# Kernel tuning notes

Measured on AMD Instinct MI355X. Metric: run time of the kernel, lower is better.

Reference implementation:

```python
import jax, jax.numpy as jnp
import numpy as np

# Config (matches init_kwargs)
B, T, N = 32, 512, 1024
FT, FS = 16, 32                 # max_time_F, max_space_F
NCH = FT * FS                   # n_channels = 512
MULT = 2
DIN = NCH * MULT                # input_dim = 1024
H = 1024                        # hidden_size
NCLS = 1                        # n_cls_tokens
NP = (T // FT) * (N // FS)      # n_patches = 1024
SCALE = float(H) ** 0.5         # config.scale is None -> hidden_size**0.5


def setup_inputs() -> dict:
    key = jax.random.key(0)
    k0, k1, k2, k3 = jax.random.split(key, 4)
    s = 0.02
    return {
        "spikes": jax.random.normal(k0, (B, T, N), dtype=jnp.float32),
        "W_embed": jax.random.normal(k1, (DIN, NCH), dtype=jnp.float32) * s,
        "b_embed": jnp.zeros((DIN,), dtype=jnp.float32),
        "cls_tokens": jnp.zeros((1, NCLS, DIN), dtype=jnp.float32),
        "W_proj": jax.random.normal(k2, (H, DIN), dtype=jnp.float32) * s,
        "b_proj": jnp.zeros((H,), dtype=jnp.float32),
        "pos_table": jax.random.normal(k3, (NP + NCLS, H), dtype=jnp.float32) * s,
    }


def reference(spikes, W_embed, b_embed, cls_tokens, W_proj, b_proj, pos_table):
    Bsz = spikes.shape[0]
    # Patchify: replaces the double python loop with one reshape/transpose.
    # [B,T,N] -> [B, T/FT, FT, N/FS, FS] -> [B, T/FT, N/FS, FT, FS] -> [B, NP, NCH]
    # flatten order (time-major within patch) matches torch's .flatten(1) on [B,FT,FS].
    patches = spikes.reshape(Bsz, T // FT, FT, N // FS, FS)
    patches = patches.transpose(0, 1, 3, 2, 4).reshape(Bsz, NP, NCH)
    # embed_spikes (linear)
    x = jnp.einsum("bpc,dc->bpd", patches, W_embed) + b_embed
    # prepend cls tokens
    cls = jnp.broadcast_to(cls_tokens, (Bsz, NCLS, DIN))
    x = jnp.concatenate([cls, x], axis=1)
    # act * scale, then projection
    x = jax.nn.gelu(x, approximate=False) * SCALE
    x = jnp.einsum("bpd,hd->bph", x, W_proj) + b_proj
    # positional embedding: stamps are arange, so direct table add
    stamp = jnp.broadcast_to(
        jnp.arange(NP + NCLS, dtype=jnp.int32)[None, :], (Bsz, NP + NCLS)
    )
    mask = jnp.ones((Bsz, NP + NCLS), dtype=jnp.int32)
    x = x + pos_table[None, :, :]
    # dropout p=0.0 -> identity
    return (x, mask, stamp)
```

## Files before the change

### kernel.cpp

```cpp
#include <hip/hip_runtime.h>
#include <stdint.h>


typedef __attribute__((ext_vector_type(8))) short bf16x8;
typedef __attribute__((ext_vector_type(4))) float f32x4;

#define VMCNT(n) asm volatile("s_waitcnt vmcnt(" #n ")" ::: "memory")
#define CFENCE() asm volatile("" ::: "memory")

__device__ __forceinline__ unsigned short f2bf(float f) {
  union { float f; unsigned u; } v; v.f = f;
  const unsigned u = v.u;
  return (unsigned short)((u + 0x7fffu + ((u >> 16) & 1u)) >> 16);
}

__device__ __forceinline__ float gelu_exact(float x) {
  return 0.5f * x * (1.0f + erff(x * 0.70710678118654752440f));
}

__device__ __forceinline__ void gl_lds16(const unsigned short* g, unsigned short* l) {
  __builtin_amdgcn_global_load_lds(
      (const __attribute__((address_space(1))) unsigned int*)g,
      (__attribute__((address_space(3))) unsigned int*)l, 16, 0, 0);
}


__global__ void cast_f32_bf16(const float* __restrict__ src,
                              unsigned short* __restrict__ dst, int n) {
  const int i = blockIdx.x * 256 + threadIdx.x;
  if (i < n) dst[i] = f2bf(src[i]);
}

__global__ void patchify(const float* __restrict__ spikes,
                         unsigned short* __restrict__ P) {
  const int idx = blockIdx.x * 256 + threadIdx.x;
  const int m = idx >> 7;
  const int c = (idx & 127) << 2;
  const int b = m >> 10, p = m & 1023;
  const int pt = p >> 5, ps = p & 31;
  const int ft = c >> 5, fs = c & 31;
  const float4 v = *(const float4*)(spikes +
      (size_t)(((b << 9) + pt * 16 + ft) << 10) + ps * 32 + fs);
  ushort4 o;
  o.x = f2bf(v.x); o.y = f2bf(v.y); o.z = f2bf(v.z); o.w = f2bf(v.w);
  *(ushort4*)(P + (size_t)m * 512 + c) = o;
}

__global__ void g0_and_pad(const float* __restrict__ cls,
                           unsigned short* __restrict__ G) {
  const int i = blockIdx.x * 256 + threadIdx.x;
  G[(size_t)32800 * 1024 + i] = 0;
  if (i < 1024) {
    const unsigned short bv = f2bf(gelu_exact(cls[i]) * 32.0f);
    for (int b = 0; b < 32; ++b) G[(size_t)(b * 1025) * 1024 + i] = bv;
  }
}

__global__ void mask_stamp(float* __restrict__ out) {
  const int i = blockIdx.x * 256 + threadIdx.x;
  if (i < 32800) {
    out[33587200 + i] = 1.0f;
    out[33587200 + 32800 + i] = (float)(i % 1025);
  }
}

__device__ __forceinline__ void stage_tile(
    const unsigned short* __restrict__ A, const unsigned short* __restrict__ B,
    int K, int rowStart, int colStart, int k0, int g0,
    unsigned short* la, unsigned short* lb) {
#pragma unroll
  for (int s = 0; s < 4; ++s) {
    const int g = g0 + s * 64;
    const int r = g >> 3;
    const int slot = g & 7;
    const int kc = (slot ^ (r & 7)) << 3;
    gl_lds16(A + (size_t)(rowStart + r) * K + (k0 + kc), la + r * 64 + slot * 8);
    gl_lds16(B + (size_t)(colStart + r) * K + (k0 + kc), lb + r * 64 + slot * 8);
  }
}

template <int K, bool GELU_EPI, int ROWBLKS>
__global__ __launch_bounds__(256) void gemm_bt(
    const unsigned short* __restrict__ A, const unsigned short* __restrict__ B,
    const float* __restrict__ bias, unsigned short* __restrict__ Cg,
    float* __restrict__ Cf, const float* __restrict__ pos, int Mvalid) {
  __shared__ __align__(16) unsigned short lsA[2][128 * 64];
  __shared__ __align__(16) unsigned short lsB[2][128 * 64];
  constexpr int NT = K / 64;

  const int tid = threadIdx.x;
  const int lane = tid & 63;
  const int w = tid >> 6;
  const int quad = lane >> 4;
  const int l16 = lane & 15;

  const int L = blockIdx.x;
  const int xcd = L & 7;
  const int j = L >> 3;
  int rowBlk, colBlk;
  if (ROWBLKS > 256 && j >= 256) { rowBlk = 256; colBlk = xcd; }
  else { rowBlk = xcd * 32 + (j >> 3); colBlk = j & 7; }
  const int rowStart = rowBlk * 128;
  const int colStart = colBlk * 128;
  const int wm = (w >> 1) * 64;
  const int wn = (w & 1) * 64;

  f32x4 acc[4][4];
  const f32x4 z = {0.f, 0.f, 0.f, 0.f};
#pragma unroll
  for (int i = 0; i < 4; ++i)
#pragma unroll
    for (int j2 = 0; j2 < 4; ++j2) acc[i][j2] = z;

  const int g0 = w * 256 + lane;

  stage_tile(A, B, K, rowStart, colStart, 0, g0, lsA[0], lsB[0]);

  for (int t = 0; t < NT; ++t) {
    const int cur = t & 1;
    if (t + 1 < NT) {
      stage_tile(A, B, K, rowStart, colStart, (t + 1) * 64, g0,
                 lsA[cur ^ 1], lsB[cur ^ 1]);
      VMCNT(8);
    } else {
      VMCNT(0);
    }
    __builtin_amdgcn_s_barrier();
    CFENCE();

    const unsigned short* cA = lsA[cur];
    const unsigned short* cB = lsB[cur];
#pragma unroll
    for (int kk = 0; kk < 64; kk += 32) {
      bf16x8 af[4], bfr[4];
      const int kcb = (kk >> 3) + quad;
#pragma unroll
      for (int i = 0; i < 4; ++i) {
        const int r = wm + i * 16 + l16;
        af[i] = *(const bf16x8*)(cA + r * 64 + ((kcb ^ (r & 7)) << 3));
      }
#pragma unroll
      for (int j2 = 0; j2 < 4; ++j2) {
        const int r = wn + j2 * 16 + l16;
        bfr[j2] = *(const bf16x8*)(cB + r * 64 + ((kcb ^ (r & 7)) << 3));
      }
#pragma unroll
      for (int i = 0; i < 4; ++i)
#pragma unroll
        for (int j2 = 0; j2 < 4; ++j2)
          acc[i][j2] = __builtin_amdgcn_mfma_f32_16x16x32_bf16(af[i], bfr[j2],
                                                               acc[i][j2], 0, 0, 0);
    }

    CFENCE();
    __builtin_amdgcn_s_barrier();
    CFENCE();
  }

#pragma unroll
  for (int i = 0; i < 4; ++i) {
    const int rb = rowStart + wm + i * 16 + quad * 4;
#pragma unroll
    for (int j2 = 0; j2 < 4; ++j2) {
      const int gc = colStart + wn + j2 * 16 + l16;
      const float bv = bias[gc];
#pragma unroll
      for (int r = 0; r < 4; ++r) {
        const int row = rb + r;
        float v = acc[i][j2][r] + bv;
        if (GELU_EPI) {
          v = gelu_exact(v) * 32.0f;
          const int grow = row + (row >> 10) + 1;
          Cg[(size_t)grow * 1024 + gc] = f2bf(v);
        } else {
          if (row < Mvalid) {
            const int p = row % 1025;
            Cf[(size_t)row * 1024 + gc] = v + pos[(size_t)p * 1024 + gc];
          }
        }
      }
    }
  }
}


extern "C" void kernel_launch(void* const* d_in, const int* in_sizes, int n_in,
                              void* d_out, int out_size, void* d_ws, size_t ws_size,
                              hipStream_t stream) {
  const float* spikes  = (const float*)d_in[0];
  const float* W_embed = (const float*)d_in[1];
  const float* b_embed = (const float*)d_in[2];
  const float* cls     = (const float*)d_in[3];
  const float* W_proj  = (const float*)d_in[4];
  const float* b_proj  = (const float*)d_in[5];
  const float* pos     = (const float*)d_in[6];
  float* out = (float*)d_out;

  char* ws = (char*)d_ws;
  unsigned short* P  = (unsigned short*)(ws);
  unsigned short* G  = (unsigned short*)(ws + 33554432);
  unsigned short* WE = (unsigned short*)(ws + 100925440);
  unsigned short* WP = (unsigned short*)(ws + 101974016);

  hipLaunchKernelGGL(cast_f32_bf16, dim3(2048), dim3(256), 0, stream, W_embed, WE, 524288);
  hipLaunchKernelGGL(cast_f32_bf16, dim3(4096), dim3(256), 0, stream, W_proj, WP, 1048576);
  hipLaunchKernelGGL(patchify, dim3(16384), dim3(256), 0, stream, spikes, P);
  hipLaunchKernelGGL(g0_and_pad, dim3(384), dim3(256), 0, stream, cls, G);
  hipLaunchKernelGGL(mask_stamp, dim3(129), dim3(256), 0, stream, out);

  hipLaunchKernelGGL((gemm_bt<512, true, 256>), dim3(2048), dim3(256), 0, stream,
                     P, WE, b_embed, G, (float*)nullptr, (const float*)nullptr, 0);
  hipLaunchKernelGGL((gemm_bt<1024, false, 257>), dim3(2056), dim3(256), 0, stream,
                     G, WP, b_proj, (unsigned short*)nullptr, out, pos, 32800);
}
```

Before: 419.9 us.

## Enlarge GEMM tiles to 256x256 with 512-thread blocks and XCD-aware mapping

Both GEMMs now use 256x256 output tiles computed by 8 waves of 512 threads, each wave holding a 128x64 accumulator. The grid shrinks to about 512 blocks, and a new XCD-contiguous work-id mapping replaces the fixed row/column block decode. Out-of-range A rows are clamped to rmax. The larger tiles are meant to raise arithmetic intensity and LDS reuse per global load. In exchange, LDS use doubles to 128KB per block and register pressure rises, which may limit occupancy to one block per CU and leaves a coarse wave tail on 256 CUs.

```diff
diff --git a/kernel.cpp b/kernel.cpp
--- a/kernel.cpp
+++ b/kernel.cpp
@@ -64,28 +64,31 @@
   }
 }
 
-__device__ __forceinline__ void stage_tile(
+__device__ __forceinline__ void stage_tile256(
     const unsigned short* __restrict__ A, const unsigned short* __restrict__ B,
-    int K, int rowStart, int colStart, int k0, int g0,
+    int K, int rowStart, int colStart, int rmax, int k0, int tid,
     unsigned short* la, unsigned short* lb) {
 #pragma unroll
-  for (int s = 0; s < 4; ++s) {
-    const int g = g0 + s * 64;
+  for (int l = 0; l < 4; ++l) {
+    const int g = l * 512 + tid;
     const int r = g >> 3;
     const int slot = g & 7;
     const int kc = (slot ^ (r & 7)) << 3;
-    gl_lds16(A + (size_t)(rowStart + r) * K + (k0 + kc), la + r * 64 + slot * 8);
-    gl_lds16(B + (size_t)(colStart + r) * K + (k0 + kc), lb + r * 64 + slot * 8);
-  }
-}
-
-template <int K, bool GELU_EPI, int ROWBLKS>
-__global__ __launch_bounds__(256) void gemm_bt(
+    int ra = rowStart + r;
+    if (ra > rmax) ra = rmax;
+    gl_lds16(A + (size_t)ra * K + (k0 + kc), la + g * 8);
+    gl_lds16(B + (size_t)(colStart + r) * K + (k0 + kc), lb + g * 8);
+  }
+}
+
+template <int K, bool GELU_EPI>
+__global__ __launch_bounds__(512, 2) void gemm_bt(
     const unsigned short* __restrict__ A, const unsigned short* __restrict__ B,
     const float* __restrict__ bias, unsigned short* __restrict__ Cg,
-    float* __restrict__ Cf, const float* __restrict__ pos, int Mvalid) {
-  __shared__ __align__(16) unsigned short lsA[2][128 * 64];
-  __shared__ __align__(16) unsigned short lsB[2][128 * 64];
+    float* __restrict__ Cf, const float* __restrict__ pos,
+    int Mvalid, int rmax, int nRowBlk) {
+  __shared__ __align__(16) unsigned short lsA[2][16384];
+  __shared__ __align__(16) unsigned short lsB[2][16384];
   constexpr int NT = K / 64;
 
   const int tid = threadIdx.x;
@@ -93,34 +96,36 @@
   const int w = tid >> 6;
   const int quad = lane >> 4;
   const int l16 = lane & 15;
-
-  const int L = blockIdx.x;
-  const int xcd = L & 7;
-  const int j = L >> 3;
-  int rowBlk, colBlk;
-  if (ROWBLKS > 256 && j >= 256) { rowBlk = 256; colBlk = xcd; }
-  else { rowBlk = xcd * 32 + (j >> 3); colBlk = j & 7; }
-  const int rowStart = rowBlk * 128;
-  const int colStart = colBlk * 128;
-  const int wm = (w >> 1) * 64;
-  const int wn = (w & 1) * 64;
-
-  f32x4 acc[4][4];
+  const int wm = (w >> 2) * 128;
+  const int wn = (w & 3) * 64;
+
+  const int nwg = nRowBlk * 4;
+  const int q = nwg >> 3, rr = nwg & 7;
+  const int xcd = blockIdx.x & 7, jj = blockIdx.x >> 3;
+  const int wgid =
+      (xcd < rr ? xcd * (q + 1) : rr * (q + 1) + (xcd - rr) * q) + jj;
+  const int rowStart = (wgid >> 2) << 8;
+  const int colStart = (wgid & 3) << 8;
+
+  f32x4 acc[8][4];
   const f32x4 z = {0.f, 0.f, 0.f, 0.f};
 #pragma unroll
-  for (int i = 0; i < 4; ++i)
-#pragma unroll
-    for (int j2 = 0; j2 < 4; ++j2) acc[i][j2] = z;
-
-  const int g0 = w * 256 + lane;
-
-  stage_tile(A, B, K, rowStart, colStart, 0, g0, lsA[0], lsB[0]);
+  for (int i = 0; i < 8; ++i)
+#pragma unroll
+    for (int j = 0; j < 4; ++j) acc[i][j] = z;
+
+  stage_tile256(A, B, K, rowStart, colStart, rmax, 0, tid, lsA[0], lsB[0]);
+
+  const int aoff = (wm + l16) << 6;
+  const int boff = (wn + l16) << 6;
+  const int sl0 = (quad ^ (l16 & 7)) << 3;
+  const int sl1 = ((4 + quad) ^ (l16 & 7)) << 3;
 
   for (int t = 0; t < NT; ++t) {
     const int cur = t & 1;
     if (t + 1 < NT) {
-      stage_tile(A, B, K, rowStart, colStart, (t + 1) * 64, g0,
-                 lsA[cur ^ 1], lsB[cur ^ 1]);
+      stage_tile256(A, B, K, rowStart, colStart, rmax, (t + 1) * 64, tid,
+                    lsA[cur ^ 1], lsB[cur ^ 1]);
       VMCNT(8);
     } else {
       VMCNT(0);
@@ -130,26 +135,36 @@
 
     const unsigned short* cA = lsA[cur];
     const unsigned short* cB = lsB[cur];
-#pragma unroll
-    for (int kk = 0; kk < 64; kk += 32) {
-      bf16x8 af[4], bfr[4];
-      const int kcb = (kk >> 3) + quad;
-#pragma unroll
-      for (int i = 0; i < 4; ++i) {
-        const int r = wm + i * 16 + l16;
-        af[i] = *(const bf16x8*)(cA + r * 64 + ((kcb ^ (r & 7)) << 3));
-      }
-#pragma unroll
-      for (int j2 = 0; j2 < 4; ++j2) {
-        const int r = wn + j2 * 16 + l16;
-        bfr[j2] = *(const bf16x8*)(cB + r * 64 + ((kcb ^ (r & 7)) << 3));
-      }
-#pragma unroll
-      for (int i = 0; i < 4; ++i)
-#pragma unroll
-        for (int j2 = 0; j2 < 4; ++j2)
-          acc[i][j2] = __builtin_amdgcn_mfma_f32_16x16x32_bf16(af[i], bfr[j2],
-                                                               acc[i][j2], 0, 0, 0);
+
+    {
+      bf16x8 af[8], bf[4];
+#pragma unroll
+      for (int i = 0; i < 8; ++i)
+        af[i] = *(const bf16x8*)(cA + aoff + i * 1024 + sl0);
+#pragma unroll
+      for (int j = 0; j < 4; ++j)
+        bf[j] = *(const bf16x8*)(cB + boff + j * 1024 + sl0);
+#pragma unroll
+      for (int i = 0; i < 8; ++i)
+#pragma unroll
+        for (int j = 0; j < 4; ++j)
+          acc[i][j] = __builtin_amdgcn_mfma_f32_16x16x32_bf16(af[i], bf[j],
+                                                              acc[i][j], 0, 0, 0);
+    }
+    {
+      bf16x8 af[8], bf[4];
+#pragma unroll
+      for (int i = 0; i < 8; ++i)
+        af[i] = *(const bf16x8*)(cA + aoff + i * 1024 + sl1);
+#pragma unroll
+      for (int j = 0; j < 4; ++j)
+        bf[j] = *(const bf16x8*)(cB + boff + j * 1024 + sl1);
+#pragma unroll
+      for (int i = 0; i < 8; ++i)
+#pragma unroll
+        for (int j = 0; j < 4; ++j)
+          acc[i][j] = __builtin_amdgcn_mfma_f32_16x16x32_bf16(af[i], bf[j],
+                                                              acc[i][j], 0, 0, 0);
     }
 
     CFENCE();
@@ -158,16 +173,16 @@
   }
 
 #pragma unroll
-  for (int i = 0; i < 4; ++i) {
+  for (int i = 0; i < 8; ++i) {
     const int rb = rowStart + wm + i * 16 + quad * 4;
 #pragma unroll
-    for (int j2 = 0; j2 < 4; ++j2) {
-      const int gc = colStart + wn + j2 * 16 + l16;
+    for (int j = 0; j < 4; ++j) {
+      const int gc = colStart + wn + j * 16 + l16;
       const float bv = bias[gc];
 #pragma unroll
       for (int r = 0; r < 4; ++r) {
         const int row = rb + r;
-        float v = acc[i][j2][r] + bv;
+        float v = acc[i][j][r] + bv;
         if (GELU_EPI) {
           v = gelu_exact(v) * 32.0f;
           const int grow = row + (row >> 10) + 1;
@@ -208,8 +223,10 @@
   hipLaunchKernelGGL(g0_and_pad, dim3(384), dim3(256), 0, stream, cls, G);
   hipLaunchKernelGGL(mask_stamp, dim3(129), dim3(256), 0, stream, out);
 
-  hipLaunchKernelGGL((gemm_bt<512, true, 256>), dim3(2048), dim3(256), 0, stream,
-                     P, WE, b_embed, G, (float*)nullptr, (const float*)nullptr, 0);
-  hipLaunchKernelGGL((gemm_bt<1024, false, 257>), dim3(2056), dim3(256), 0, stream,
-                     G, WP, b_proj, (unsigned short*)nullptr, out, pos, 32800);
-}
+  hipLaunchKernelGGL((gemm_bt<512, true>), dim3(512), dim3(512), 0, stream,
+                     P, WE, b_embed, G, (float*)nullptr, (const float*)nullptr,
+                     0, 32767, 128);
+  hipLaunchKernelGGL((gemm_bt<1024, false>), dim3(516), dim3(512), 0, stream,
+                     G, WP, b_proj, (unsigned short*)nullptr, out, pos,
+                     32800, 32895, 129);
+}
```

After: 477.9 us. 13.8% more time.

## Fuse patchify and bf16 cast into first GEMM's A-tile loading

Applied to the files above, without the earlier changes.

Removes the separate patchify kernel and its 32 MB bf16 intermediate. The first GEMM now reads fp32 spikes directly through registers, converts them to bf16 and stores them into swizzled LDS, while B still uses direct global-to-LDS loads. This saves a full write and read of the patch matrix plus one launch. In exchange the A path goes through registers, with an added barrier and a full vmcnt wait per iteration, which may reduce overlap inside the GEMM.

```diff
diff --git a/kernel.cpp b/kernel.cpp
--- a/kernel.cpp
+++ b/kernel.cpp
@@ -6,6 +6,7 @@
 typedef __attribute__((ext_vector_type(4))) float f32x4;
 
 #define VMCNT(n) asm volatile("s_waitcnt vmcnt(" #n ")" ::: "memory")
+#define LGKM0()  asm volatile("s_waitcnt lgkmcnt(0)" ::: "memory")
 #define CFENCE() asm volatile("" ::: "memory")
 
 __device__ __forceinline__ unsigned short f2bf(float f) {
@@ -29,21 +30,6 @@
                               unsigned short* __restrict__ dst, int n) {
   const int i = blockIdx.x * 256 + threadIdx.x;
   if (i < n) dst[i] = f2bf(src[i]);
-}
-
-__global__ void patchify(const float* __restrict__ spikes,
-                         unsigned short* __restrict__ P) {
-  const int idx = blockIdx.x * 256 + threadIdx.x;
-  const int m = idx >> 7;
-  const int c = (idx & 127) << 2;
-  const int b = m >> 10, p = m & 1023;
-  const int pt = p >> 5, ps = p & 31;
-  const int ft = c >> 5, fs = c & 31;
-  const float4 v = *(const float4*)(spikes +
-      (size_t)(((b << 9) + pt * 16 + ft) << 10) + ps * 32 + fs);
-  ushort4 o;
-  o.x = f2bf(v.x); o.y = f2bf(v.y); o.z = f2bf(v.z); o.w = f2bf(v.w);
-  *(ushort4*)(P + (size_t)m * 512 + c) = o;
 }
 
 __global__ void g0_and_pad(const float* __restrict__ cls,
@@ -64,9 +50,144 @@
   }
 }
 
-__device__ __forceinline__ void stage_tile(
+__global__ __launch_bounds__(256) void gemm1_fused(
+    const float* __restrict__ spikes, const unsigned short* __restrict__ Bw,
+    const float* __restrict__ bias, unsigned short* __restrict__ G) {
+  __shared__ __align__(16) unsigned short lsA[2][8192];
+  __shared__ __align__(16) unsigned short lsB[2][8192];
+  const int tid = threadIdx.x;
+  const int lane = tid & 63;
+  const int w = tid >> 6;
+  const int quad = lane >> 4;
+  const int l16 = lane & 15;
+
+  const int L = blockIdx.x;
+  const int xcd = L & 7;
+  const int j = L >> 3;
+  const int rowBlk = xcd * 32 + (j >> 3), colBlk = j & 7;
+  const int rowStart = rowBlk * 128;
+  const int colStart = colBlk * 128;
+  const int wm = (w >> 1) * 64;
+  const int wn = (w & 1) * 64;
+
+  f32x4 acc[4][4];
+  const f32x4 z = {0.f, 0.f, 0.f, 0.f};
+#pragma unroll
+  for (int i = 0; i < 4; ++i)
+#pragma unroll
+    for (int j2 = 0; j2 < 4; ++j2) acc[i][j2] = z;
+
+  const int g0 = w * 256 + lane;
+  unsigned aoff[4];
+  int bRow[4], bKc[4], ldsOff[4];
+#pragma unroll
+  for (int s = 0; s < 4; ++s) {
+    const int g = g0 + s * 64, r = g >> 3, slot = g & 7;
+    const int m = rowStart + r, b = m >> 10, p = m & 1023;
+    const int pt = p >> 5, ps = p & 31;
+    const int chunk = slot ^ (r & 7);
+    aoff[s] = (unsigned)((((b << 9) + (pt << 4) + (chunk >> 2)) << 10) +
+                         (ps << 5) + ((chunk & 3) << 3));
+    bRow[s] = colStart + r;
+    bKc[s] = chunk << 3;
+    ldsOff[s] = g * 8;
+  }
+
+  float4 ar[8];
+#pragma unroll
+  for (int s = 0; s < 4; ++s) {
+    const float* sp = spikes + aoff[s];
+    ar[2 * s] = *(const float4*)(sp);
+    ar[2 * s + 1] = *(const float4*)(sp + 4);
+    gl_lds16(Bw + (size_t)bRow[s] * 512 + bKc[s], lsB[0] + ldsOff[s]);
+  }
+  VMCNT(0);
+#pragma unroll
+  for (int s = 0; s < 4; ++s) {
+    union { unsigned short u[8]; bf16x8 v; } pk;
+    pk.u[0] = f2bf(ar[2 * s].x); pk.u[1] = f2bf(ar[2 * s].y);
+    pk.u[2] = f2bf(ar[2 * s].z); pk.u[3] = f2bf(ar[2 * s].w);
+    pk.u[4] = f2bf(ar[2 * s + 1].x); pk.u[5] = f2bf(ar[2 * s + 1].y);
+    pk.u[6] = f2bf(ar[2 * s + 1].z); pk.u[7] = f2bf(ar[2 * s + 1].w);
+    *(bf16x8*)(lsA[0] + ldsOff[s]) = pk.v;
+  }
+  LGKM0();
+  CFENCE(); __builtin_amdgcn_s_barrier(); CFENCE();
+
+  for (int t = 0; t < 8; ++t) {
+    const int cur = t & 1;
+    const bool pf = (t < 7);
+    if (pf) {
+#pragma unroll
+      for (int s = 0; s < 4; ++s) {
+        const float* sp = spikes + aoff[s] + (unsigned)(t + 1) * 2048u;
+        ar[2 * s] = *(const float4*)(sp);
+        ar[2 * s + 1] = *(const float4*)(sp + 4);
+        gl_lds16(Bw + (size_t)bRow[s] * 512 + ((t + 1) << 6) + bKc[s],
+                 lsB[cur ^ 1] + ldsOff[s]);
+      }
+    }
+
+    const unsigned short* cA = lsA[cur];
+    const unsigned short* cB = lsB[cur];
+#pragma unroll
+    for (int kk = 0; kk < 64; kk += 32) {
+      bf16x8 af[4], bfr[4];
+      const int kcb = (kk >> 3) + quad;
+#pragma unroll
+      for (int i = 0; i < 4; ++i) {
+        const int r = wm + i * 16 + l16;
+        af[i] = *(const bf16x8*)(cA + r * 64 + ((kcb ^ (r & 7)) << 3));
+      }
+#pragma unroll
+      for (int j2 = 0; j2 < 4; ++j2) {
+        const int r = wn + j2 * 16 + l16;
+        bfr[j2] = *(const bf16x8*)(cB + r * 64 + ((kcb ^ (r & 7)) << 3));
+      }
+#pragma unroll
+      for (int i = 0; i < 4; ++i)
+#pragma unroll
+        for (int j2 = 0; j2 < 4; ++j2)
+          acc[i][j2] = __builtin_amdgcn_mfma_f32_16x16x32_bf16(af[i], bfr[j2],
+                                                               acc[i][j2], 0, 0, 0);
+    }
+
+    CFENCE(); __builtin_amdgcn_s_barrier(); CFENCE();
+    if (pf) {
+      VMCNT(0);
+#pragma unroll
+      for (int s = 0; s < 4; ++s) {
+        union { unsigned short u[8]; bf16x8 v; } pk;
+        pk.u[0] = f2bf(ar[2 * s].x); pk.u[1] = f2bf(ar[2 * s].y);
+        pk.u[2] = f2bf(ar[2 * s].z); pk.u[3] = f2bf(ar[2 * s].w);
+        pk.u[4] = f2bf(ar[2 * s + 1].x); pk.u[5] = f2bf(ar[2 * s + 1].y);
+        pk.u[6] = f2bf(ar[2 * s + 1].z); pk.u[7] = f2bf(ar[2 * s + 1].w);
+        *(bf16x8*)(lsA[cur ^ 1] + ldsOff[s]) = pk.v;
+      }
+      LGKM0();
+    }
+    CFENCE(); __builtin_amdgcn_s_barrier(); CFENCE();
+  }
+
+  float bv[4];
+#pragma unroll
+  for (int j2 = 0; j2 < 4; ++j2) bv[j2] = bias[colStart + wn + j2 * 16 + l16];
+#pragma unroll
+  for (int i = 0; i < 4; ++i)
+#pragma unroll
+    for (int r2 = 0; r2 < 4; ++r2) {
+      const int row = rowStart + wm + i * 16 + quad * 4 + r2;
+      const int grow = row + (row >> 10) + 1;
+      unsigned short* go = G + (size_t)grow * 1024 + colStart + wn + l16;
+#pragma unroll
+      for (int j2 = 0; j2 < 4; ++j2)
+        go[j2 * 16] = f2bf(gelu_exact(acc[i][j2][r2] + bv[j2]) * 32.0f);
+    }
+}
+
+__device__ __forceinline__ void stage_tile2(
     const unsigned short* __restrict__ A, const unsigned short* __restrict__ B,
-    int K, int rowStart, int colStart, int k0, int g0,
+    int rowStart, int colStart, int k0, int g0,
     unsigned short* la, unsigned short* lb) {
 #pragma unroll
   for (int s = 0; s < 4; ++s) {
@@ -74,20 +195,17 @@
     const int r = g >> 3;
     const int slot = g & 7;
     const int kc = (slot ^ (r & 7)) << 3;
-    gl_lds16(A + (size_t)(rowStart + r) * K + (k0 + kc), la + r * 64 + slot * 8);
-    gl_lds16(B + (size_t)(colStart + r) * K + (k0 + kc), lb + r * 64 + slot * 8);
-  }
-}
-
-template <int K, bool GELU_EPI, int ROWBLKS>
-__global__ __launch_bounds__(256) void gemm_bt(
+    gl_lds16(A + (size_t)(rowStart + r) * 1024 + (k0 + kc), la + g * 8);
+    gl_lds16(B + (size_t)(colStart + r) * 1024 + (k0 + kc), lb + g * 8);
+  }
+}
+
+__global__ __launch_bounds__(256) void gemm2_bt(
     const unsigned short* __restrict__ A, const unsigned short* __restrict__ B,
-    const float* __restrict__ bias, unsigned short* __restrict__ Cg,
-    float* __restrict__ Cf, const float* __restrict__ pos, int Mvalid) {
-  __shared__ __align__(16) unsigned short lsA[2][128 * 64];
-  __shared__ __align__(16) unsigned short lsB[2][128 * 64];
-  constexpr int NT = K / 64;
-
+    const float* __restrict__ bias, float* __restrict__ Cf,
+    const float* __restrict__ pos, int Mvalid) {
+  __shared__ __align__(16) unsigned short lsA[2][8192];
+  __shared__ __align__(16) unsigned short lsB[2][8192];
   const int tid = threadIdx.x;
   const int lane = tid & 63;
   const int w = tid >> 6;
@@ -98,7 +216,7 @@
   const int xcd = L & 7;
   const int j = L >> 3;
   int rowBlk, colBlk;
-  if (ROWBLKS > 256 && j >= 256) { rowBlk = 256; colBlk = xcd; }
+  if (j >= 256) { rowBlk = 256; colBlk = xcd; }
   else { rowBlk = xcd * 32 + (j >> 3); colBlk = j & 7; }
   const int rowStart = rowBlk * 128;
   const int colStart = colBlk * 128;
@@ -113,14 +231,13 @@
     for (int j2 = 0; j2 < 4; ++j2) acc[i][j2] = z;
 
   const int g0 = w * 256 + lane;
-
-  stage_tile(A, B, K, rowStart, colStart, 0, g0, lsA[0], lsB[0]);
-
-  for (int t = 0; t < NT; ++t) {
+  stage_tile2(A, B, rowStart, colStart, 0, g0, lsA[0], lsB[0]);
+
+  for (int t = 0; t < 16; ++t) {
     const int cur = t & 1;
-    if (t + 1 < NT) {
-      stage_tile(A, B, K, rowStart, colStart, (t + 1) * 64, g0,
-                 lsA[cur ^ 1], lsB[cur ^ 1]);
+    if (t + 1 < 16) {
+      stage_tile2(A, B, rowStart, colStart, (t + 1) * 64, g0,
+                  lsA[cur ^ 1], lsB[cur ^ 1]);
       VMCNT(8);
     } else {
       VMCNT(0);
@@ -157,30 +274,23 @@
     CFENCE();
   }
 
-#pragma unroll
-  for (int i = 0; i < 4; ++i) {
-    const int rb = rowStart + wm + i * 16 + quad * 4;
-#pragma unroll
-    for (int j2 = 0; j2 < 4; ++j2) {
-      const int gc = colStart + wn + j2 * 16 + l16;
-      const float bv = bias[gc];
-#pragma unroll
-      for (int r = 0; r < 4; ++r) {
-        const int row = rb + r;
-        float v = acc[i][j2][r] + bv;
-        if (GELU_EPI) {
-          v = gelu_exact(v) * 32.0f;
-          const int grow = row + (row >> 10) + 1;
-          Cg[(size_t)grow * 1024 + gc] = f2bf(v);
-        } else {
-          if (row < Mvalid) {
-            const int p = row % 1025;
-            Cf[(size_t)row * 1024 + gc] = v + pos[(size_t)p * 1024 + gc];
-          }
-        }
-      }
-    }
-  }
+  float bv[4];
+#pragma unroll
+  for (int j2 = 0; j2 < 4; ++j2) bv[j2] = bias[colStart + wn + j2 * 16 + l16];
+#pragma unroll
+  for (int i = 0; i < 4; ++i)
+#pragma unroll
+    for (int r2 = 0; r2 < 4; ++r2) {
+      const int row = rowStart + wm + i * 16 + quad * 4 + r2;
+      if (row < Mvalid) {
+        const int p = row % 1025;
+        const float* pr = pos + (size_t)p * 1024 + colStart + wn + l16;
+        float* co = Cf + (size_t)row * 1024 + colStart + wn + l16;
+#pragma unroll
+        for (int j2 = 0; j2 < 4; ++j2)
+          co[j2 * 16] = acc[i][j2][r2] + bv[j2] + pr[j2 * 16];
+      }
+    }
 }
 
 
@@ -197,19 +307,17 @@
   float* out = (float*)d_out;
 
   char* ws = (char*)d_ws;
-  unsigned short* P  = (unsigned short*)(ws);
   unsigned short* G  = (unsigned short*)(ws + 33554432);
   unsigned short* WE = (unsigned short*)(ws + 100925440);
   unsigned short* WP = (unsigned short*)(ws + 101974016);
 
   hipLaunchKernelGGL(cast_f32_bf16, dim3(2048), dim3(256), 0, stream, W_embed, WE, 524288);
   hipLaunchKernelGGL(cast_f32_bf16, dim3(4096), dim3(256), 0, stream, W_proj, WP, 1048576);
-  hipLaunchKernelGGL(patchify, dim3(16384), dim3(256), 0, stream, spikes, P);
   hipLaunchKernelGGL(g0_and_pad, dim3(384), dim3(256), 0, stream, cls, G);
   hipLaunchKernelGGL(mask_stamp, dim3(129), dim3(256), 0, stream, out);
 
-  hipLaunchKernelGGL((gemm_bt<512, true, 256>), dim3(2048), dim3(256), 0, stream,
-                     P, WE, b_embed, G, (float*)nullptr, (const float*)nullptr, 0);
-  hipLaunchKernelGGL((gemm_bt<1024, false, 257>), dim3(2056), dim3(256), 0, stream,
-                     G, WP, b_proj, (unsigned short*)nullptr, out, pos, 32800);
-}
+  hipLaunchKernelGGL(gemm1_fused, dim3(2048), dim3(256), 0, stream,
+                     spikes, WE, b_embed, G);
+  hipLaunchKernelGGL(gemm2_bt, dim3(2056), dim3(256), 0, stream,
+                     G, WP, b_proj, out, pos, 32800);
+}
```

Measured after the change: 397.3 us. 5.4% less time.
